# Optimization experiments

Measured on AMD Instinct MI355X. Metric: run time of the kernel, lower is better.

Reference implementation:

```python
import jax, jax.numpy as jnp
import numpy as np

MAX_DELTAS = 4
PACK = 8  # 4-bit values packed into int32
HIDDEN = 4096
Q_SLICE = 4096   # num_heads(32) * head_size(128)
KV_SLICE = 1024  # num_kv_heads(8) * head_size(128)
TOKENS = 4096


def setup_inputs() -> dict:
    key = jax.random.key(0)
    ks = jax.random.split(key, 16)
    imax = 2**31 - 1
    inp = {
        "x": jax.random.normal(ks[0], (TOKENS, HIDDEN), dtype=jnp.float32),
        "base_weight": jax.random.normal(ks[1], (Q_SLICE + 2 * KV_SLICE, HIDDEN), dtype=jnp.float32) * 0.02,
        "qweight_q": jax.random.randint(ks[2], (MAX_DELTAS, 1, HIDDEN // PACK, Q_SLICE), 0, imax, dtype=jnp.int32),
        "qweight_k": jax.random.randint(ks[3], (MAX_DELTAS, 1, HIDDEN // PACK, KV_SLICE), 0, imax, dtype=jnp.int32),
        "qweight_v": jax.random.randint(ks[4], (MAX_DELTAS, 1, HIDDEN // PACK, KV_SLICE), 0, imax, dtype=jnp.int32),
        "qzeros_q": jax.random.randint(ks[5], (MAX_DELTAS, 1, 1, Q_SLICE // PACK), 0, imax, dtype=jnp.int32),
        "qzeros_k": jax.random.randint(ks[6], (MAX_DELTAS, 1, 1, KV_SLICE // PACK), 0, imax, dtype=jnp.int32),
        "qzeros_v": jax.random.randint(ks[7], (MAX_DELTAS, 1, 1, KV_SLICE // PACK), 0, imax, dtype=jnp.int32),
        "scales_q": jax.random.uniform(ks[8], (MAX_DELTAS, 1, 1, Q_SLICE), dtype=jnp.float32) * 0.01,
        "scales_k": jax.random.uniform(ks[9], (MAX_DELTAS, 1, 1, KV_SLICE), dtype=jnp.float32) * 0.01,
        "scales_v": jax.random.uniform(ks[10], (MAX_DELTAS, 1, 1, KV_SLICE), dtype=jnp.float32) * 0.01,
        "indices": jax.random.randint(ks[11], (TOKENS,), 0, MAX_DELTAS, dtype=jnp.int32),
    }
    return inp


def _unpack_rows(qw):
    # (D, 1, K//PACK, N) int32 -> (D, K, N) 4-bit values, packed along K
    D, _, Kp, N = qw.shape
    shifts = (jnp.arange(PACK, dtype=jnp.int32) * 4)
    q = (qw[:, 0, :, None, :] >> shifts[None, None, :, None]) & 0xF  # (D,Kp,PACK,N)
    return q.reshape(D, Kp * PACK, N)


def _unpack_cols(qz):
    # (D, 1, 1, N//PACK) int32 -> (D, N), packed along N
    D = qz.shape[0]
    shifts = (jnp.arange(PACK, dtype=jnp.int32) * 4)
    z = (qz[:, 0, 0, :, None] >> shifts[None, None, :]) & 0xF  # (D, N//PACK, PACK)
    return z.reshape(D, -1)


def _dequant(qw, qz, sc):
    # GPTQ-style dequant, single group (g_idx is all zeros): W = (q - (z+1)) * scale
    q = _unpack_rows(qw).astype(jnp.float32)            # (D, K, N)
    z = (_unpack_cols(qz) + 1).astype(jnp.float32)      # (D, N)
    return (q - z[:, None, :]) * sc[:, 0, 0, :][:, None, :]


def _delta_slice(x, indices, qw, qz, sc):
    # per-token indexed delta matmul: out[t] = x[t] @ W[indices[t]] (0 if index==-1)
    W = _dequant(qw, qz, sc)  # (D, K, N)
    out = jnp.zeros((x.shape[0], W.shape[2]), dtype=x.dtype)
    for d in range(MAX_DELTAS):
        mask = (indices == d).astype(x.dtype)[:, None]
        out = out + (x * mask) @ W[d]
    return out


def reference(x, base_weight, qweight_q, qweight_k, qweight_v,
              qzeros_q, qzeros_k, qzeros_v,
              scales_q, scales_k, scales_v, indices):
    # base merged QKV projection
    base_out = x @ base_weight.T  # (T, q + 2*kv)
    # per-slice delta adds (offsets handled by concatenation order: q, k, v)
    dq = _delta_slice(x, indices, qweight_q, qzeros_q, scales_q)
    dk = _delta_slice(x, indices, qweight_k, qzeros_k, scales_k)
    dv = _delta_slice(x, indices, qweight_v, qzeros_v, scales_v)
    return base_out + jnp.concatenate([dq, dk, dv], axis=1)
```

## Files before the change

kernel.cpp:

```cpp
#include <hip/hip_runtime.h>
#include <stdint.h>

#define TOKENS 4096
#define HIDDEN 4096
#define NQ     4096
#define NKV    1024
#define NTOT   6144
#define KPACK  512
#define MAXTILES 36

typedef __attribute__((ext_vector_type(8))) __bf16 bf16x8;
typedef __attribute__((ext_vector_type(8))) short short8v;
typedef __attribute__((ext_vector_type(4))) float floatx4;

__device__ __forceinline__ short f2bf(float f) {
  union { float f; unsigned u; } v; v.f = f;
  unsigned r = v.u + 0x7fffu + ((v.u >> 16) & 1u);
  return (short)(r >> 16);
}
__device__ __forceinline__ float bf2f(short s) {
  union { float f; unsigned u; } v; v.u = ((unsigned)(unsigned short)s) << 16;
  return v.f;
}

__device__ __forceinline__ void load_lds16(const void* g, void* l) {
  __builtin_amdgcn_global_load_lds((__attribute__((address_space(1))) void*)(g),
                                   (__attribute__((address_space(3))) void*)(l),
                                   16, 0, 0);
}

__global__ __launch_bounds__(256) void prep_tokens(const int* __restrict__ idx,
                                                   int* __restrict__ token_list,
                                                   int* __restrict__ grp) {
  __shared__ int cnt[4], cur[4];
  const int tid = threadIdx.x;
  if (tid < 4) cnt[tid] = 0;
  __syncthreads();
  for (int t = tid; t < TOKENS; t += 256) {
    int d = idx[t];
    if ((unsigned)d < 4u) atomicAdd(&cnt[d], 1);
  }
  __syncthreads();
  if (tid == 0) {
    int s = 0, nt = 0;
    for (int d = 0; d < 4; d++) {
      cur[d] = s; grp[d] = s; grp[4 + d] = cnt[d]; s += cnt[d];
      int tiles = (cnt[d] + 127) >> 7;
      for (int rt = 0; rt < tiles; rt++) grp[9 + nt++] = d | (rt << 2);
    }
    grp[8] = nt;
  }
  __syncthreads();
  for (int t = tid; t < TOKENS; t += 256) {
    int d = idx[t];
    if ((unsigned)d < 4u) {
      int p = atomicAdd(&cur[d], 1);
      token_list[p] = t;
    }
  }
}

__global__ __launch_bounds__(256) void cvt_x(const float* __restrict__ x,
                                             short* __restrict__ xb) {
  size_t g = (size_t)blockIdx.x * 256 + threadIdx.x;
  size_t i = g * 8;
  float4 a = ((const float4*)(x + i))[0];
  float4 b = ((const float4*)(x + i))[1];
  short8v o;
  o[0] = f2bf(a.x); o[1] = f2bf(a.y); o[2] = f2bf(a.z); o[3] = f2bf(a.w);
  o[4] = f2bf(b.x); o[5] = f2bf(b.y); o[6] = f2bf(b.z); o[7] = f2bf(b.w);
  *(short8v*)(xb + i) = o;
}

__global__ __launch_bounds__(256) void combine_w(
    const float* __restrict__ bw,
    const int* __restrict__ qwq, const int* __restrict__ qwk, const int* __restrict__ qwv,
    const int* __restrict__ qzq, const int* __restrict__ qzk, const int* __restrict__ qzv,
    const float* __restrict__ scq, const float* __restrict__ sck, const float* __restrict__ scv,
    short* __restrict__ wc) {
  __shared__ short tile[4][64][72];
  __shared__ float zs[4][64], ss[4][64];
  const int tid = threadIdx.x;
  const int n0  = blockIdx.y * 64;
  const int kp0 = blockIdx.x * 8;

  const int* qw; const int* qz; const float* sc; int Ns, nb;
  if (n0 < NQ)            { qw = qwq; qz = qzq; sc = scq; Ns = NQ;  nb = n0; }
  else if (n0 < NQ + NKV) { qw = qwk; qz = qzk; sc = sck; Ns = NKV; nb = n0 - NQ; }
  else                    { qw = qwv; qz = qzv; sc = scv; Ns = NKV; nb = n0 - NQ - NKV; }

  {
    int d = tid >> 6, n = tid & 63;
    int nn = nb + n;
    int z = (int)(((unsigned)qz[d * (Ns >> 3) + (nn >> 3)] >> ((nn & 7) * 4)) & 0xFu);
    zs[d][n] = (float)(z + 1);
    ss[d][n] = sc[d * Ns + nn];
  }
  __syncthreads();

#pragma unroll
  for (int d = 0; d < 4; d++) {
#pragma unroll
    for (int p = 0; p < 2; p++) {
      int i  = tid + p * 256;
      int kp = i >> 6, n = i & 63;
      unsigned q32 = (unsigned)qw[((size_t)d * KPACK + kp0 + kp) * Ns + nb + n];
      float z = zs[d][n], s = ss[d][n];
      short8v o;
#pragma unroll
      for (int j = 0; j < 8; j++)
        o[j] = f2bf(((float)((q32 >> (4 * j)) & 0xFu) - z) * s);
      *(short8v*)&tile[d][n][kp * 8] = o;
    }
  }
  __syncthreads();

  const int kl = (tid & 7) * 8;
#pragma unroll
  for (int p = 0; p < 2; p++) {
    int n = (tid >> 3) + p * 32;
    const float4* bp = (const float4*)(bw + (size_t)(n0 + n) * HIDDEN + kp0 * 8 + kl);
    float4 b0 = bp[0], b1 = bp[1];
    float bv[8] = {b0.x, b0.y, b0.z, b0.w, b1.x, b1.y, b1.z, b1.w};
#pragma unroll
    for (int d = 0; d < 4; d++) {
      short8v w = *(short8v*)&tile[d][n][kl];
      short8v o;
#pragma unroll
      for (int j = 0; j < 8; j++) o[j] = f2bf(bv[j] + bf2f(w[j]));
      *(short8v*)(wc + ((size_t)d * NTOT + n0 + n) * HIDDEN + kp0 * 8 + kl) = o;
    }
  }
}

__global__ __launch_bounds__(256) void gemm_grouped(
    const short* __restrict__ xb, const short* __restrict__ wc,
    const int* __restrict__ token_list, const int* __restrict__ grp,
    float* __restrict__ out) {
  const int nt = grp[8];
  if ((int)blockIdx.y >= nt) return;
  const int te = grp[9 + blockIdx.y];
  const int d  = te & 3;
  const int rt = te >> 2;
  const int cnt   = grp[4 + d];
  const int start = grp[d];
  const int n0 = blockIdx.x * 128;

  __shared__ __align__(16) short As[128 * 32];
  __shared__ __align__(16) short Bs[128 * 32];
  __shared__ int toks[128];

  const int tid = threadIdx.x;
  if (tid < 128) {
    int r = rt * 128 + tid;
    if (r >= cnt) r = cnt - 1;
    toks[tid] = token_list[start + r];
  }
  __syncthreads();

  const int wave = tid >> 6;
  const int lane = tid & 63;

  const int u0  = wave * 128 + lane;
  const int rA0 = u0 >> 2;
  const int sw  = ((lane & 3) ^ ((lane >> 3) & 3)) * 8;

  const short* gA0 = xb + (size_t)toks[rA0] * HIDDEN + sw;
  const short* gA1 = xb + (size_t)toks[rA0 + 16] * HIDDEN + sw;
  const short* wrow = wc + ((size_t)d * NTOT + n0) * HIDDEN;
  const short* gB0 = wrow + (size_t)rA0 * HIDDEN + sw;
  const short* gB1 = gB0 + 16 * HIDDEN;
  short* lA0 = As + (size_t)wave * 1024;
  short* lA1 = lA0 + 512;
  short* lB0 = Bs + (size_t)wave * 1024;
  short* lB1 = lB0 + 512;

  const int mrow = lane & 15;
  const int sx  = (((lane >> 4) ^ ((mrow >> 1) & 3))) * 8;
  const int wm  = (wave >> 1) * 64;
  const int wn  = (wave & 1) * 64;

  floatx4 acc[4][4];
#pragma unroll
  for (int i = 0; i < 4; i++)
#pragma unroll
    for (int j = 0; j < 4; j++) acc[i][j] = (floatx4){0.f, 0.f, 0.f, 0.f};

  for (int k0 = 0; k0 < HIDDEN; k0 += 32) {
    load_lds16(gA0 + k0, lA0);
    load_lds16(gA1 + k0, lA1);
    load_lds16(gB0 + k0, lB0);
    load_lds16(gB1 + k0, lB1);
    __syncthreads();

    bf16x8 a[4], b[4];
#pragma unroll
    for (int i = 0; i < 4; i++)
      a[i] = *(const bf16x8*)(As + (wm + i * 16 + mrow) * 32 + sx);
#pragma unroll
    for (int j = 0; j < 4; j++)
      b[j] = *(const bf16x8*)(Bs + (wn + j * 16 + mrow) * 32 + sx);
#pragma unroll
    for (int i = 0; i < 4; i++)
#pragma unroll
      for (int j = 0; j < 4; j++)
        acc[i][j] = __builtin_amdgcn_mfma_f32_16x16x32_bf16(a[i], b[j], acc[i][j], 0, 0, 0);
    __syncthreads();
  }

  const int rbase = (lane >> 4) * 4;
  const int coll  = lane & 15;
#pragma unroll
  for (int i = 0; i < 4; i++) {
#pragma unroll
    for (int r = 0; r < 4; r++) {
      int m = wm + i * 16 + rbase + r;
      if (rt * 128 + m < cnt) {
        float* orow = out + (size_t)toks[m] * NTOT + n0 + wn + coll;
#pragma unroll
        for (int j = 0; j < 4; j++) orow[j * 16] = acc[i][j][r];
      }
    }
  }
}

extern "C" void kernel_launch(void* const* d_in, const int* in_sizes, int n_in,
                              void* d_out, int out_size, void* d_ws, size_t ws_size,
                              hipStream_t stream) {
  const float* x   = (const float*)d_in[0];
  const float* bw  = (const float*)d_in[1];
  const int*   qwq = (const int*)d_in[2];
  const int*   qwk = (const int*)d_in[3];
  const int*   qwv = (const int*)d_in[4];
  const int*   qzq = (const int*)d_in[5];
  const int*   qzk = (const int*)d_in[6];
  const int*   qzv = (const int*)d_in[7];
  const float* scq = (const float*)d_in[8];
  const float* sck = (const float*)d_in[9];
  const float* scv = (const float*)d_in[10];
  const int*   idx = (const int*)d_in[11];
  float* out = (float*)d_out;

  char* ws = (char*)d_ws;
  short* xb = (short*)ws;
  short* wc = (short*)(ws + (size_t)33554432);
  int* token_list = (int*)(ws + (size_t)33554432 + 201326592);
  int* grp = token_list + TOKENS;

  prep_tokens<<<1, 256, 0, stream>>>(idx, token_list, grp);
  cvt_x<<<(TOKENS * HIDDEN) / (256 * 8), 256, 0, stream>>>(x, xb);
  dim3 gc(HIDDEN / 64, NTOT / 64);
  combine_w<<<gc, 256, 0, stream>>>(bw, qwq, qwk, qwv, qzq, qzk, qzv, scq, sck, scv, wc);
  dim3 gg(NTOT / 128, MAXTILES);
  gemm_grouped<<<gg, 256, 0, stream>>>(xb, wc, token_list, grp, out);
}
```

Baseline: 709.1 us.

## Widen GEMM tile to 128x256 and simplify weight-combine dequant staging

```diff
diff --git a/kernel.cpp b/kernel.cpp
--- a/kernel.cpp
+++ b/kernel.cpp
@@ -17,10 +17,6 @@
   union { float f; unsigned u; } v; v.f = f;
   unsigned r = v.u + 0x7fffu + ((v.u >> 16) & 1u);
   return (short)(r >> 16);
-}
-__device__ __forceinline__ float bf2f(short s) {
-  union { float f; unsigned u; } v; v.u = ((unsigned)(unsigned short)s) << 16;
-  return v.f;
 }
 
 __device__ __forceinline__ void load_lds16(const void* g, void* l) {
@@ -78,7 +74,7 @@
     const int* __restrict__ qzq, const int* __restrict__ qzk, const int* __restrict__ qzv,
     const float* __restrict__ scq, const float* __restrict__ sck, const float* __restrict__ scv,
     short* __restrict__ wc) {
-  __shared__ short tile[4][64][72];
+  __shared__ int ldsq[4][8][72];
   __shared__ float zs[4][64], ss[4][64];
   const int tid = threadIdx.x;
   const int n0  = blockIdx.y * 64;
@@ -96,7 +92,6 @@
     zs[d][n] = (float)(z + 1);
     ss[d][n] = sc[d * Ns + nn];
   }
-  __syncthreads();
 
 #pragma unroll
   for (int d = 0; d < 4; d++) {
@@ -104,36 +99,32 @@
     for (int p = 0; p < 2; p++) {
       int i  = tid + p * 256;
       int kp = i >> 6, n = i & 63;
-      unsigned q32 = (unsigned)qw[((size_t)d * KPACK + kp0 + kp) * Ns + nb + n];
+      ldsq[d][kp][n] = qw[((size_t)d * KPACK + kp0 + kp) * Ns + nb + n];
+    }
+  }
+  __syncthreads();
+
+  const int kp = tid & 7;
+#pragma unroll
+  for (int p = 0; p < 2; p++) {
+    int n = (tid >> 3) + p * 32;
+    const float4* bp = (const float4*)(bw + (size_t)(n0 + n) * HIDDEN + (kp0 + kp) * 8);
+    float4 b0 = bp[0], b1 = bp[1];
+    float bv[8] = {b0.x, b0.y, b0.z, b0.w, b1.x, b1.y, b1.z, b1.w};
+#pragma unroll
+    for (int d = 0; d < 4; d++) {
+      unsigned q32 = (unsigned)ldsq[d][kp][n];
       float z = zs[d][n], s = ss[d][n];
       short8v o;
 #pragma unroll
       for (int j = 0; j < 8; j++)
-        o[j] = f2bf(((float)((q32 >> (4 * j)) & 0xFu) - z) * s);
-      *(short8v*)&tile[d][n][kp * 8] = o;
-    }
-  }
-  __syncthreads();
-
-  const int kl = (tid & 7) * 8;
-#pragma unroll
-  for (int p = 0; p < 2; p++) {
-    int n = (tid >> 3) + p * 32;
-    const float4* bp = (const float4*)(bw + (size_t)(n0 + n) * HIDDEN + kp0 * 8 + kl);
-    float4 b0 = bp[0], b1 = bp[1];
-    float bv[8] = {b0.x, b0.y, b0.z, b0.w, b1.x, b1.y, b1.z, b1.w};
-#pragma unroll
-    for (int d = 0; d < 4; d++) {
-      short8v w = *(short8v*)&tile[d][n][kl];
-      short8v o;
-#pragma unroll
-      for (int j = 0; j < 8; j++) o[j] = f2bf(bv[j] + bf2f(w[j]));
-      *(short8v*)(wc + ((size_t)d * NTOT + n0 + n) * HIDDEN + kp0 * 8 + kl) = o;
-    }
-  }
-}
-
-__global__ __launch_bounds__(256) void gemm_grouped(
+        o[j] = f2bf(((float)((q32 >> (4 * j)) & 0xFu) - z) * s + bv[j]);
+      *(short8v*)(wc + ((size_t)d * NTOT + n0 + n) * HIDDEN + (kp0 + kp) * 8) = o;
+    }
+  }
+}
+
+__global__ __launch_bounds__(256, 2) void gemm_grouped(
     const short* __restrict__ xb, const short* __restrict__ wc,
     const int* __restrict__ token_list, const int* __restrict__ grp,
     float* __restrict__ out) {
@@ -144,10 +135,10 @@
   const int rt = te >> 2;
   const int cnt   = grp[4 + d];
   const int start = grp[d];
-  const int n0 = blockIdx.x * 128;
+  const int n0 = blockIdx.x * 256;
 
   __shared__ __align__(16) short As[128 * 32];
-  __shared__ __align__(16) short Bs[128 * 32];
+  __shared__ __align__(16) short Bs[256 * 32];
   __shared__ int toks[128];
 
   const int tid = threadIdx.x;
@@ -161,49 +152,56 @@
   const int wave = tid >> 6;
   const int lane = tid & 63;
 
-  const int u0  = wave * 128 + lane;
-  const int rA0 = u0 >> 2;
-  const int sw  = ((lane & 3) ^ ((lane >> 3) & 3)) * 8;
-
-  const short* gA0 = xb + (size_t)toks[rA0] * HIDDEN + sw;
-  const short* gA1 = xb + (size_t)toks[rA0 + 16] * HIDDEN + sw;
-  const short* wrow = wc + ((size_t)d * NTOT + n0) * HIDDEN;
-  const short* gB0 = wrow + (size_t)rA0 * HIDDEN + sw;
-  const short* gB1 = gB0 + 16 * HIDDEN;
+  const int sw = ((lane & 3) ^ ((lane >> 3) & 3)) * 8;
+
+  const int arow0 = wave * 32 + (lane >> 2);
+  const short* gA0 = xb + (size_t)toks[arow0] * HIDDEN + sw;
+  const short* gA1 = xb + (size_t)toks[arow0 + 16] * HIDDEN + sw;
   short* lA0 = As + (size_t)wave * 1024;
   short* lA1 = lA0 + 512;
-  short* lB0 = Bs + (size_t)wave * 1024;
+
+  const short* wrow = wc + ((size_t)d * NTOT + n0) * HIDDEN;
+  const int brow0 = wave * 64 + (lane >> 2);
+  const short* gB0 = wrow + (size_t)brow0 * HIDDEN + sw;
+  const short* gB1 = gB0 + (size_t)16 * HIDDEN;
+  const short* gB2 = gB0 + (size_t)32 * HIDDEN;
+  const short* gB3 = gB0 + (size_t)48 * HIDDEN;
+  short* lB0 = Bs + (size_t)wave * 2048;
   short* lB1 = lB0 + 512;
+  short* lB2 = lB0 + 1024;
+  short* lB3 = lB0 + 1536;
 
   const int mrow = lane & 15;
-  const int sx  = (((lane >> 4) ^ ((mrow >> 1) & 3))) * 8;
-  const int wm  = (wave >> 1) * 64;
-  const int wn  = (wave & 1) * 64;
-
-  floatx4 acc[4][4];
+  const int sx = (((lane >> 4) ^ ((mrow >> 1) & 3))) * 8;
+  const int wm = (wave >> 1) * 64;
+  const int wn = (wave & 1) * 128;
+
+  floatx4 acc[4][8];
 #pragma unroll
   for (int i = 0; i < 4; i++)
 #pragma unroll
-    for (int j = 0; j < 4; j++) acc[i][j] = (floatx4){0.f, 0.f, 0.f, 0.f};
+    for (int j = 0; j < 8; j++) acc[i][j] = (floatx4){0.f, 0.f, 0.f, 0.f};
 
   for (int k0 = 0; k0 < HIDDEN; k0 += 32) {
     load_lds16(gA0 + k0, lA0);
     load_lds16(gA1 + k0, lA1);
     load_lds16(gB0 + k0, lB0);
     load_lds16(gB1 + k0, lB1);
+    load_lds16(gB2 + k0, lB2);
+    load_lds16(gB3 + k0, lB3);
     __syncthreads();
 
-    bf16x8 a[4], b[4];
+    bf16x8 a[4], b[8];
 #pragma unroll
     for (int i = 0; i < 4; i++)
       a[i] = *(const bf16x8*)(As + (wm + i * 16 + mrow) * 32 + sx);
 #pragma unroll
-    for (int j = 0; j < 4; j++)
+    for (int j = 0; j < 8; j++)
       b[j] = *(const bf16x8*)(Bs + (wn + j * 16 + mrow) * 32 + sx);
 #pragma unroll
     for (int i = 0; i < 4; i++)
 #pragma unroll
-      for (int j = 0; j < 4; j++)
+      for (int j = 0; j < 8; j++)
         acc[i][j] = __builtin_amdgcn_mfma_f32_16x16x32_bf16(a[i], b[j], acc[i][j], 0, 0, 0);
     __syncthreads();
   }
@@ -218,7 +216,7 @@
       if (rt * 128 + m < cnt) {
         float* orow = out + (size_t)toks[m] * NTOT + n0 + wn + coll;
 #pragma unroll
-        for (int j = 0; j < 4; j++) orow[j * 16] = acc[i][j][r];
+        for (int j = 0; j < 8; j++) orow[j * 16] = acc[i][j][r];
       }
     }
   }
@@ -251,6 +249,6 @@
   cvt_x<<<(TOKENS * HIDDEN) / (256 * 8), 256, 0, stream>>>(x, xb);
   dim3 gc(HIDDEN / 64, NTOT / 64);
   combine_w<<<gc, 256, 0, stream>>>(bw, qwq, qwk, qwv, qzq, qzk, qzv, scq, sck, scv, wc);
-  dim3 gg(NTOT / 128, MAXTILES);
+  dim3 gg(NTOT / 256, MAXTILES);
   gemm_grouped<<<gg, 256, 0, stream>>>(xb, wc, token_list, grp, out);
 }
```

Result: faster. 583.9 us (-17.7%).
